# Optimization experiments

Hardware: AMD Instinct MI355X
Metric: run time of the kernel (lower is better)

Reference implementation:

```python
import jax, jax.numpy as jnp
import numpy as np

EMB = 64
N_NODES = 50000
N_EDGES = 800000

def _mlp(h, W1, b1, W2, b2):
    h = jax.nn.relu(h @ W1 + b1)
    return jax.nn.relu(h @ W2 + b2)

def setup_inputs() -> dict:
    key = jax.random.key(0)
    ks = jax.random.split(key, 12)
    s = 1.0 / np.sqrt(3 * EMB)
    s2 = 1.0 / np.sqrt(EMB)
    x = jax.random.normal(ks[0], (N_NODES, 2 * EMB), dtype=jnp.float32)
    edge_index = jax.random.randint(ks[1], (2, N_EDGES), 0, N_NODES, dtype=jnp.int32)
    edge_attr = jax.random.normal(ks[2], (N_EDGES, EMB), dtype=jnp.float32)
    u = jax.random.normal(ks[3], (64, 64), dtype=jnp.float32)
    batch = jax.random.randint(ks[4], (N_NODES,), 0, 64, dtype=jnp.int32)
    W1a = jax.random.uniform(ks[5], (3 * EMB, EMB), jnp.float32, -s, s)
    b1a = jax.random.uniform(ks[6], (EMB,), jnp.float32, -s, s)
    W1b = jax.random.uniform(ks[7], (EMB, EMB), jnp.float32, -s2, s2)
    b1b = jax.random.uniform(ks[8], (EMB,), jnp.float32, -s2, s2)
    W2a = jax.random.uniform(ks[9], (3 * EMB, EMB), jnp.float32, -s, s)
    b2a = jax.random.uniform(ks[10], (EMB,), jnp.float32, -s, s)
    W2b = jax.random.uniform(ks[11], (EMB, EMB), jnp.float32, -s2, s2)
    b2b = jax.random.uniform(jax.random.fold_in(key, 99), (EMB,), jnp.float32, -s2, s2)
    return {"x": x, "edge_index": edge_index, "edge_attr": edge_attr, "u": u, "batch": batch,
            "W1a": W1a, "b1a": b1a, "W1b": W1b, "b1b": b1b,
            "W2a": W2a, "b2a": b2a, "W2b": W2b, "b2b": b2b}

def reference(x, edge_index, edge_attr, u, batch, W1a, b1a, W1b, b1b, W2a, b2a, W2b, b2b):
    senders, receivers = edge_index[0], edge_index[1]
    # gather sender node features [E, 2*EMB] and concat edge features -> [E, 3*EMB]
    msg = jnp.concatenate([x[senders], edge_attr], axis=1)
    msg = _mlp(msg, W1a, b1a, W1b, b1b)  # [E, EMB]
    agg = jax.ops.segment_sum(msg, receivers, num_segments=x.shape[0])  # [N, EMB]
    h = jnp.concatenate([x, agg], axis=1)  # [N, 3*EMB]
    return _mlp(h, W2a, b2a, W2b, b2b)  # [N, EMB]
```

## Files before the change

kernel.cpp:

```cpp
#include <hip/hip_runtime.h>
#include <hip/hip_bf16.h>

typedef __attribute__((ext_vector_type(8))) __bf16 bf16x8;
typedef __attribute__((ext_vector_type(4))) __bf16 bf16x4;
typedef __attribute__((ext_vector_type(2))) __bf16 bf16x2;
typedef __attribute__((ext_vector_type(4))) float f32x4;

#define MFMA(a, b, c) __builtin_amdgcn_mfma_f32_16x16x32_bf16((a), (b), (c), 0, 0, 0)

__device__ __forceinline__ bf16x8 pack8(f32x4 a, f32x4 b) {
    bf16x8 r;
    r[0] = (__bf16)a[0]; r[1] = (__bf16)a[1]; r[2] = (__bf16)a[2]; r[3] = (__bf16)a[3];
    r[4] = (__bf16)b[0]; r[5] = (__bf16)b[1]; r[6] = (__bf16)b[2]; r[7] = (__bf16)b[3];
    return r;
}

__device__ __forceinline__ bf16x8 cvt8(const float* __restrict__ p) {
    return pack8(*(const f32x4*)(p), *(const f32x4*)(p + 4));
}

__global__ __launch_bounds__(256) void zero_i32(int* __restrict__ p, int n) {
    for (int i = blockIdx.x * blockDim.x + threadIdx.x; i < n;
         i += gridDim.x * blockDim.x)
        p[i] = 0;
}

__global__ __launch_bounds__(256) void precompute_y(
    const float* __restrict__ x,
    const float* __restrict__ W1a, const float* __restrict__ b1a,
    const float* __restrict__ W2a, const float* __restrict__ b2a,
    float* __restrict__ y1, float* __restrict__ y2,
    int N, int ntiles)
{
    const int LDK = 136;
    __shared__ __align__(16) __bf16 w1t[64 * 136];
    __shared__ __align__(16) __bf16 w2t[64 * 136];
    for (int idx = threadIdx.x; idx < 64 * 128; idx += 256) {
        int k = idx >> 6, n = idx & 63;
        w1t[n * LDK + k] = (__bf16)W1a[k * 64 + n];
        w2t[n * LDK + k] = (__bf16)W2a[k * 64 + n];
    }
    __syncthreads();

    const int lane = threadIdx.x & 63, wave = threadIdx.x >> 6;
    const int l15 = lane & 15, l4 = lane >> 4;

    f32x4 bias1[4], bias2[4];
#pragma unroll
    for (int nt = 0; nt < 4; ++nt) {
        bias1[nt] = *(const f32x4*)(b1a + nt * 16 + l4 * 4);
        bias2[nt] = *(const f32x4*)(b2a + nt * 16 + l4 * 4);
    }

    for (int tile = blockIdx.x * 4 + wave; tile < ntiles; tile += gridDim.x * 4) {
        const int node = tile * 16 + l15;
        const int nrow = min(node, N - 1);
        f32x4 acc1[4], acc2[4];
#pragma unroll
        for (int nt = 0; nt < 4; ++nt) {
            acc1[nt] = (f32x4){0.f, 0.f, 0.f, 0.f};
            acc2[nt] = (f32x4){0.f, 0.f, 0.f, 0.f};
        }
#pragma unroll
        for (int j = 0; j < 4; ++j) {
            const int k0 = j * 32 + l4 * 8;
            bf16x8 b = cvt8(x + (size_t)nrow * 128 + k0);
#pragma unroll
            for (int nt = 0; nt < 4; ++nt) {
                bf16x8 a1 = *(const bf16x8*)(w1t + (nt * 16 + l15) * LDK + k0);
                acc1[nt] = MFMA(a1, b, acc1[nt]);
                bf16x8 a2 = *(const bf16x8*)(w2t + (nt * 16 + l15) * LDK + k0);
                acc2[nt] = MFMA(a2, b, acc2[nt]);
            }
        }
        if (node < N) {
#pragma unroll
            for (int nt = 0; nt < 4; ++nt) {
                f32x4 v1 = acc1[nt] + bias1[nt];
                f32x4 v2 = acc2[nt] + bias2[nt];
                *(f32x4*)(y1 + (size_t)node * 64 + nt * 16 + l4 * 4) = v1;
                *(f32x4*)(y2 + (size_t)node * 64 + nt * 16 + l4 * 4) = v2;
            }
        }
    }
}

__global__ __launch_bounds__(256) void hist_rank(
    const int* __restrict__ recv, int* __restrict__ cnt,
    int* __restrict__ rank, int E)
{
    for (int e = blockIdx.x * blockDim.x + threadIdx.x; e < E;
         e += gridDim.x * blockDim.x)
        rank[e] = atomicAdd(&cnt[recv[e]], 1);
}

__global__ __launch_bounds__(1024) void scan_offsets(
    const int* __restrict__ cnt, int* __restrict__ offs, int N)
{
    __shared__ int wsum[16];
    __shared__ int stot;
    const int tid = threadIdx.x;
    const int lane = tid & 63, wave = tid >> 6;
    int carry = 0;
    const int CH = 4096;
    for (int base = 0; base < N; base += CH) {
        const int idx = base + tid * 4;
        int v0 = (idx + 0 < N) ? cnt[idx + 0] : 0;
        int v1 = (idx + 1 < N) ? cnt[idx + 1] : 0;
        int v2 = (idx + 2 < N) ? cnt[idx + 2] : 0;
        int v3 = (idx + 3 < N) ? cnt[idx + 3] : 0;
        const int t = v0 + v1 + v2 + v3;
        int s = t;
#pragma unroll
        for (int d = 1; d < 64; d <<= 1) {
            int u = __shfl_up(s, d);
            if (lane >= d) s += u;
        }
        if (lane == 63) wsum[wave] = s;
        __syncthreads();
        if (wave == 0) {
            int w = (lane < 16) ? wsum[lane] : 0;
            int ws = w;
#pragma unroll
            for (int d = 1; d < 16; d <<= 1) {
                int u = __shfl_up(ws, d);
                if (lane >= d) ws += u;
            }
            if (lane < 16) wsum[lane] = ws - w;
            if (lane == 15) stot = ws;
        }
        __syncthreads();
        const int excl = s - t + wsum[wave] + carry;
        if (idx + 0 < N) offs[idx + 0] = excl;
        if (idx + 1 < N) offs[idx + 1] = excl + v0;
        if (idx + 2 < N) offs[idx + 2] = excl + v0 + v1;
        if (idx + 3 < N) offs[idx + 3] = excl + v0 + v1 + v2;
        carry += stot;
        __syncthreads();
    }
    if (tid == 0) offs[N] = carry;
}

template<int MODE>
__global__ __launch_bounds__(256) void edge_mlp(
    const float* __restrict__ eattr,
    const int* __restrict__ send, const int* __restrict__ recv,
    const int* __restrict__ rank, const int* __restrict__ offs,
    const float* __restrict__ W1a, const float* __restrict__ W1b,
    const float* __restrict__ b1b,
    const float* __restrict__ y1,
    __bf16* __restrict__ msgC, float* agg,
    int E, int ntiles)
{
    __shared__ __align__(16) __bf16 wfA[8 * 65 * 8];
    __shared__ __align__(16) __bf16 wfB[8 * 65 * 8];
    __shared__ __align__(16) __bf16 hfrag[4][8 * 17 * 8];
    for (int idx = threadIdx.x; idx < 64 * 64; idx += 256) {
        const int k = idx >> 6, n = idx & 63;
        const int c = k >> 3, i = k & 7;
        wfA[(c * 65 + n) * 8 + i] = (__bf16)W1a[(128 + k) * 64 + n];
        wfB[(c * 65 + n) * 8 + i] = (__bf16)W1b[k * 64 + n];
    }
    __syncthreads();

    const int lane = threadIdx.x & 63, wave = threadIdx.x >> 6;
    const int l15 = lane & 15, l4 = lane >> 4;
    __bf16* hf = hfrag[wave];

    f32x4 biasb[4];
#pragma unroll
    for (int nt = 0; nt < 4; ++nt) biasb[nt] = *(const f32x4*)(b1b + nt * 16 + l4 * 4);

    for (int tile = blockIdx.x * 4 + wave; tile < ntiles; tile += gridDim.x * 4) {
        const int e = tile * 16 + l15;
        const int el = min(e, E - 1);
        const int s = send[el];
        int p = 0, rv = 0;
        if (MODE == 0) {
            rv = recv[el];
            p = offs[rv] + rank[el];
        } else {
            rv = recv[el];
        }

        f32x4 acc[4];
#pragma unroll
        for (int nt = 0; nt < 4; ++nt)
            acc[nt] = *(const f32x4*)(y1 + (size_t)s * 64 + nt * 16 + l4 * 4);
#pragma unroll
        for (int j = 0; j < 2; ++j) {
            const float* ep = eattr + (size_t)el * 64 + j * 32 + l4 * 8;
            bf16x8 b = pack8(*(const f32x4*)ep, *(const f32x4*)(ep + 4));
            const int c = j * 4 + l4;
#pragma unroll
            for (int nt = 0; nt < 4; ++nt) {
                bf16x8 a = *(const bf16x8*)(wfA + ((c * 65) + nt * 16 + l15) * 8);
                acc[nt] = MFMA(a, b, acc[nt]);
            }
        }
#pragma unroll
        for (int nt = 0; nt < 4; ++nt) {
            bf16x4 hv;
#pragma unroll
            for (int r = 0; r < 4; ++r) hv[r] = (__bf16)fmaxf(acc[nt][r], 0.f);
            const int c2 = nt * 2 + (l4 >> 1);
            *(bf16x4*)(hf + (c2 * 17 + l15) * 8 + (l4 & 1) * 4) = hv;
        }
        f32x4 acc2[4];
#pragma unroll
        for (int nt = 0; nt < 4; ++nt) acc2[nt] = biasb[nt];
#pragma unroll
        for (int j = 0; j < 2; ++j) {
            const int c = j * 4 + l4;
            bf16x8 b = *(const bf16x8*)(hf + (c * 17 + l15) * 8);
#pragma unroll
            for (int nt = 0; nt < 4; ++nt) {
                bf16x8 a = *(const bf16x8*)(wfB + ((c * 65) + nt * 16 + l15) * 8);
                acc2[nt] = MFMA(a, b, acc2[nt]);
            }
        }
        if (e < E) {
            if (MODE == 0) {
                __bf16* row = msgC + (size_t)p * 64;
#pragma unroll
                for (int nt = 0; nt < 4; ++nt) {
                    bf16x4 mv;
#pragma unroll
                    for (int r = 0; r < 4; ++r) mv[r] = (__bf16)fmaxf(acc2[nt][r], 0.f);
                    *(bf16x4*)(row + nt * 16 + l4 * 4) = mv;
                }
            } else {
                float* base = agg + (size_t)rv * 64 + l4 * 4;
#pragma unroll
                for (int nt = 0; nt < 4; ++nt)
#pragma unroll
                    for (int r = 0; r < 4; ++r)
                        unsafeAtomicAdd(base + nt * 16 + r, fmaxf(acc2[nt][r], 0.f));
            }
        }
    }
}

__global__ __launch_bounds__(256) void csr_reduce(
    const unsigned* __restrict__ msg_u,
    const int* __restrict__ offs,
    __bf16* __restrict__ aggB, int N)
{
    const int wave = threadIdx.x >> 6, lane = threadIdx.x & 63;
    const int half = lane >> 5, c = lane & 31;
    for (int node = blockIdx.x * 4 + wave; node < N; node += gridDim.x * 4) {
        const int oL = offs[node], oR = offs[node + 1];
        float ax = 0.f, ay = 0.f;
        for (int p = oL + half; p < oR; p += 2) {
            const unsigned u = msg_u[(size_t)p * 32 + c];
            ax += __uint_as_float(u << 16);
            ay += __uint_as_float(u & 0xffff0000u);
        }
        ax += __shfl_xor(ax, 32);
        ay += __shfl_xor(ay, 32);
        if (half == 0) {
            bf16x2 v; v[0] = (__bf16)ax; v[1] = (__bf16)ay;
            *(bf16x2*)(aggB + (size_t)node * 64 + c * 2) = v;
        }
    }
}

template<int AGGF32>
__global__ __launch_bounds__(256) void node_pass(
    const void* __restrict__ aggp,
    const float* __restrict__ W2a, const float* __restrict__ W2b,
    const float* __restrict__ b2b,
    const float* __restrict__ y2, float* __restrict__ out,
    int N, int ntiles)
{
    const int LDK = 72;
    __shared__ __align__(16) __bf16 wat[64 * 72];
    __shared__ __align__(16) __bf16 wbt[64 * 72];
    __shared__ __align__(16) __bf16 hbuf[4][16 * 72];
    for (int idx = threadIdx.x; idx < 64 * 64; idx += 256) {
        int k = idx >> 6, n = idx & 63;
        wat[n * LDK + k] = (__bf16)W2a[(128 + k) * 64 + n];
        wbt[n * LDK + k] = (__bf16)W2b[k * 64 + n];
    }
    __syncthreads();

    const int lane = threadIdx.x & 63, wave = threadIdx.x >> 6;
    const int l15 = lane & 15, l4 = lane >> 4;
    __bf16* hb = hbuf[wave];

    f32x4 biasb[4];
#pragma unroll
    for (int nt = 0; nt < 4; ++nt) biasb[nt] = *(const f32x4*)(b2b + nt * 16 + l4 * 4);

    for (int tile = blockIdx.x * 4 + wave; tile < ntiles; tile += gridDim.x * 4) {
        const int node = tile * 16 + l15;
        const int nrow = min(node, N - 1);

        f32x4 acc[4];
#pragma unroll
        for (int nt = 0; nt < 4; ++nt)
            acc[nt] = *(const f32x4*)(y2 + (size_t)nrow * 64 + nt * 16 + l4 * 4);
#pragma unroll
        for (int j = 0; j < 2; ++j) {
            const int k0 = j * 32 + l4 * 8;
            bf16x8 b;
            if (AGGF32) b = cvt8((const float*)aggp + (size_t)nrow * 64 + k0);
            else        b = *(const bf16x8*)((const __bf16*)aggp + (size_t)nrow * 64 + k0);
#pragma unroll
            for (int nt = 0; nt < 4; ++nt) {
                bf16x8 a = *(const bf16x8*)(wat + (nt * 16 + l15) * LDK + k0);
                acc[nt] = MFMA(a, b, acc[nt]);
            }
        }
#pragma unroll
        for (int nt = 0; nt < 4; ++nt) {
            bf16x4 hv;
#pragma unroll
            for (int r = 0; r < 4; ++r) hv[r] = (__bf16)fmaxf(acc[nt][r], 0.f);
            *(bf16x4*)(hb + l15 * LDK + nt * 16 + l4 * 4) = hv;
        }

        f32x4 acc2[4];
#pragma unroll
        for (int nt = 0; nt < 4; ++nt) acc2[nt] = biasb[nt];
#pragma unroll
        for (int j = 0; j < 2; ++j) {
            const int k0 = j * 32 + l4 * 8;
            bf16x8 b = *(const bf16x8*)(hb + l15 * LDK + k0);
#pragma unroll
            for (int nt = 0; nt < 4; ++nt) {
                bf16x8 a = *(const bf16x8*)(wbt + (nt * 16 + l15) * LDK + k0);
                acc2[nt] = MFMA(a, b, acc2[nt]);
            }
        }
        if (node < N) {
#pragma unroll
            for (int nt = 0; nt < 4; ++nt) {
                f32x4 v;
#pragma unroll
                for (int r = 0; r < 4; ++r) v[r] = fmaxf(acc2[nt][r], 0.f);
                *(f32x4*)(out + (size_t)node * 64 + nt * 16 + l4 * 4) = v;
            }
        }
    }
}

extern "C" void kernel_launch(void* const* d_in, const int* in_sizes, int n_in,
                              void* d_out, int out_size, void* d_ws, size_t ws_size,
                              hipStream_t stream) {
    const float* x     = (const float*)d_in[0];
    const int*   eidx  = (const int*)d_in[1];
    const float* eattr = (const float*)d_in[2];
    const float* W1a = (const float*)d_in[5];
    const float* b1a = (const float*)d_in[6];
    const float* W1b = (const float*)d_in[7];
    const float* b1b = (const float*)d_in[8];
    const float* W2a = (const float*)d_in[9];
    const float* b2a = (const float*)d_in[10];
    const float* W2b = (const float*)d_in[11];
    const float* b2b = (const float*)d_in[12];
    float* out = (float*)d_out;

    const int N = in_sizes[0] / 128;
    const int E = in_sizes[1] / 2;
    const int* send = eidx;
    const int* recv = eidx + E;

    const size_t NG = (size_t)N * 64;
    const size_t need = 2 * NG * sizeof(float) + (size_t)E * 64 * sizeof(__bf16)
                      + ((size_t)2 * (N + 1) + E) * sizeof(int);
    const bool big = ws_size >= need;

    const int ntilesN = (N + 15) / 16;
    const int ntilesE = (E + 15) / 16;
    int blkN = (ntilesN + 3) / 4;
    if (blkN > 1024) blkN = 1024;
    int blkE = (ntilesE + 3) / 4;
    if (blkE > 1536) blkE = 1536;
    int blkS = (E + 255) / 256;
    if (blkS > 1024) blkS = 1024;
    int blkR = (N + 3) / 4;
    if (blkR > 2048) blkR = 2048;

    if (big) {
        float*  y1   = (float*)d_ws;
        float*  y2   = y1 + NG;
        __bf16* msgC = (__bf16*)(y2 + NG);
        int*    cnt  = (int*)(msgC + (size_t)E * 64);
        int*    offs = cnt + (N + 1);
        int*    rank = offs + (N + 1);
        __bf16* aggB = (__bf16*)y1;

        zero_i32<<<(N + 256) / 256, 256, 0, stream>>>(cnt, N + 1);
        hist_rank<<<blkS, 256, 0, stream>>>(recv, cnt, rank, E);
        scan_offsets<<<1, 1024, 0, stream>>>(cnt, offs, N);
        precompute_y<<<blkN, 256, 0, stream>>>(x, W1a, b1a, W2a, b2a, y1, y2, N, ntilesN);
        edge_mlp<0><<<blkE, 256, 0, stream>>>(eattr, send, recv, rank, offs,
                                              W1a, W1b, b1b, y1, msgC, nullptr, E, ntilesE);
        csr_reduce<<<blkR, 256, 0, stream>>>((const unsigned*)msgC, offs, aggB, N);
        node_pass<0><<<blkN, 256, 0, stream>>>(aggB, W2a, W2b, b2b, y2, out, N, ntilesN);
    } else {
        float* agg = (float*)d_ws;
        float* y1  = agg + NG;
        float* y2  = y1 + NG;
        zero_i32<<<2048, 256, 0, stream>>>((int*)agg, (int)NG);
        precompute_y<<<blkN, 256, 0, stream>>>(x, W1a, b1a, W2a, b2a, y1, y2, N, ntilesN);
        edge_mlp<1><<<blkE, 256, 0, stream>>>(eattr, send, recv, nullptr, nullptr,
                                              W1a, W1b, b1b, y1, nullptr, agg, E, ntilesE);
        node_pass<1><<<blkN, 256, 0, stream>>>(agg, W2a, W2b, b2b, y2, out, N, ntilesN);
    }
}
```

Measured before the change: 243.9 us.

## Store y1 as bf16, transpose hidden via shuffles, fuse CSR reduce into node MLP

Stores the precomputed sender projection y1 in bf16, using a fragment-friendly layout that halves the random-gather traffic in the edge MLP. Replaces the LDS round-trip between the two MFMA layers with register shuffles in both edge and node kernels. Fuses the CSR segment reduction into the node MLP kernel, so the separate aggregation write and read and one launch go away. The costs are extra bf16 rounding of y1, more shuffle instructions, and a serial 16-node reduction loop per wave in the fused node kernel.

Result: slower. 302.0 us (+23.8%).

```diff
diff --git a/kernel.cpp b/kernel.cpp
--- a/kernel.cpp
+++ b/kernel.cpp
@@ -5,6 +5,7 @@
 typedef __attribute__((ext_vector_type(4))) __bf16 bf16x4;
 typedef __attribute__((ext_vector_type(2))) __bf16 bf16x2;
 typedef __attribute__((ext_vector_type(4))) float f32x4;
+typedef __attribute__((ext_vector_type(4))) unsigned u32x4;
 
 #define MFMA(a, b, c) __builtin_amdgcn_mfma_f32_16x16x32_bf16((a), (b), (c), 0, 0, 0)
 
@@ -19,6 +20,36 @@
     return pack8(*(const f32x4*)(p), *(const f32x4*)(p + 4));
 }
 
+__device__ __forceinline__ unsigned pkrelu(float a, float b) {
+    unsigned short ua = __builtin_bit_cast(unsigned short, (__bf16)fmaxf(a, 0.f));
+    unsigned short ub = __builtin_bit_cast(unsigned short, (__bf16)fmaxf(b, 0.f));
+    return (unsigned)ua | ((unsigned)ub << 16);
+}
+
+__device__ __forceinline__ void transpose_h(const f32x4* acc, bf16x8* bfr,
+                                            int l15, int l4) {
+    unsigned pk[4][2];
+#pragma unroll
+    for (int nt = 0; nt < 4; ++nt) {
+        pk[nt][0] = pkrelu(acc[nt][0], acc[nt][1]);
+        pk[nt][1] = pkrelu(acc[nt][2], acc[nt][3]);
+    }
+    const int srcA = l15 + 16 * ((2 * l4) & 3);
+    const int srcB = l15 + 16 * ((2 * l4 + 1) & 3);
+    const bool hi = (l4 >> 1) != 0;
+#pragma unroll
+    for (int j = 0; j < 2; ++j) {
+        unsigned a0 = __shfl(pk[j * 2][0], srcA), a1 = __shfl(pk[j * 2][1], srcA);
+        unsigned c0 = __shfl(pk[j * 2 + 1][0], srcA), c1 = __shfl(pk[j * 2 + 1][1], srcA);
+        unsigned b0 = __shfl(pk[j * 2][0], srcB), b1 = __shfl(pk[j * 2][1], srcB);
+        unsigned d0 = __shfl(pk[j * 2 + 1][0], srcB), d1 = __shfl(pk[j * 2 + 1][1], srcB);
+        u32x4 uv;
+        uv[0] = hi ? c0 : a0; uv[1] = hi ? c1 : a1;
+        uv[2] = hi ? d0 : b0; uv[3] = hi ? d1 : b1;
+        bfr[j] = __builtin_bit_cast(bf16x8, uv);
+    }
+}
+
 __global__ __launch_bounds__(256) void zero_i32(int* __restrict__ p, int n) {
     for (int i = blockIdx.x * blockDim.x + threadIdx.x; i < n;
          i += gridDim.x * blockDim.x)
@@ -29,7 +60,7 @@
     const float* __restrict__ x,
     const float* __restrict__ W1a, const float* __restrict__ b1a,
     const float* __restrict__ W2a, const float* __restrict__ b2a,
-    float* __restrict__ y1, float* __restrict__ y2,
+    __bf16* __restrict__ y1f, float* __restrict__ y2,
     int N, int ntiles)
 {
     const int LDK = 136;
@@ -77,8 +108,11 @@
 #pragma unroll
             for (int nt = 0; nt < 4; ++nt) {
                 f32x4 v1 = acc1[nt] + bias1[nt];
+                bf16x4 bv;
+#pragma unroll
+                for (int r = 0; r < 4; ++r) bv[r] = (__bf16)v1[r];
+                *(bf16x4*)(y1f + (size_t)node * 64 + l4 * 16 + nt * 4) = bv;
                 f32x4 v2 = acc2[nt] + bias2[nt];
-                *(f32x4*)(y1 + (size_t)node * 64 + nt * 16 + l4 * 4) = v1;
                 *(f32x4*)(y2 + (size_t)node * 64 + nt * 16 + l4 * 4) = v2;
             }
         }
@@ -148,13 +182,12 @@
     const int* __restrict__ rank, const int* __restrict__ offs,
     const float* __restrict__ W1a, const float* __restrict__ W1b,
     const float* __restrict__ b1b,
-    const float* __restrict__ y1,
+    const __bf16* __restrict__ y1f,
     __bf16* __restrict__ msgC, float* agg,
     int E, int ntiles)
 {
     __shared__ __align__(16) __bf16 wfA[8 * 65 * 8];
     __shared__ __align__(16) __bf16 wfB[8 * 65 * 8];
-    __shared__ __align__(16) __bf16 hfrag[4][8 * 17 * 8];
     for (int idx = threadIdx.x; idx < 64 * 64; idx += 256) {
         const int k = idx >> 6, n = idx & 63;
         const int c = k >> 3, i = k & 7;
@@ -165,7 +198,6 @@
 
     const int lane = threadIdx.x & 63, wave = threadIdx.x >> 6;
     const int l15 = lane & 15, l4 = lane >> 4;
-    __bf16* hf = hfrag[wave];
 
     f32x4 biasb[4];
 #pragma unroll
@@ -175,18 +207,20 @@
         const int e = tile * 16 + l15;
         const int el = min(e, E - 1);
         const int s = send[el];
-        int p = 0, rv = 0;
-        if (MODE == 0) {
-            rv = recv[el];
-            p = offs[rv] + rank[el];
-        } else {
-            rv = recv[el];
-        }
-
+        const int rv = recv[el];
+        int p = 0;
+        if (MODE == 0) p = offs[rv] + rank[el];
+
+        bf16x8 cA = *(const bf16x8*)(y1f + (size_t)s * 64 + l4 * 16);
+        bf16x8 cB = *(const bf16x8*)(y1f + (size_t)s * 64 + l4 * 16 + 8);
         f32x4 acc[4];
 #pragma unroll
-        for (int nt = 0; nt < 4; ++nt)
-            acc[nt] = *(const f32x4*)(y1 + (size_t)s * 64 + nt * 16 + l4 * 4);
+        for (int r = 0; r < 4; ++r) {
+            acc[0][r] = (float)cA[r];
+            acc[1][r] = (float)cA[4 + r];
+            acc[2][r] = (float)cB[r];
+            acc[3][r] = (float)cB[4 + r];
+        }
 #pragma unroll
         for (int j = 0; j < 2; ++j) {
             const float* ep = eattr + (size_t)el * 64 + j * 32 + l4 * 8;
@@ -198,25 +232,19 @@
                 acc[nt] = MFMA(a, b, acc[nt]);
             }
         }
-#pragma unroll
-        for (int nt = 0; nt < 4; ++nt) {
-            bf16x4 hv;
-#pragma unroll
-            for (int r = 0; r < 4; ++r) hv[r] = (__bf16)fmaxf(acc[nt][r], 0.f);
-            const int c2 = nt * 2 + (l4 >> 1);
-            *(bf16x4*)(hf + (c2 * 17 + l15) * 8 + (l4 & 1) * 4) = hv;
-        }
+        bf16x8 bfr[2];
+        transpose_h(acc, bfr, l15, l4);
+
         f32x4 acc2[4];
 #pragma unroll
         for (int nt = 0; nt < 4; ++nt) acc2[nt] = biasb[nt];
 #pragma unroll
         for (int j = 0; j < 2; ++j) {
             const int c = j * 4 + l4;
-            bf16x8 b = *(const bf16x8*)(hf + (c * 17 + l15) * 8);
 #pragma unroll
             for (int nt = 0; nt < 4; ++nt) {
                 bf16x8 a = *(const bf16x8*)(wfB + ((c * 65) + nt * 16 + l15) * 8);
-                acc2[nt] = MFMA(a, b, acc2[nt]);
+                acc2[nt] = MFMA(a, bfr[j], acc2[nt]);
             }
         }
         if (e < E) {
@@ -241,52 +269,117 @@
     }
 }
 
-__global__ __launch_bounds__(256) void csr_reduce(
+__global__ __launch_bounds__(256) void node_fused(
     const unsigned* __restrict__ msg_u,
     const int* __restrict__ offs,
-    __bf16* __restrict__ aggB, int N)
-{
-    const int wave = threadIdx.x >> 6, lane = threadIdx.x & 63;
-    const int half = lane >> 5, c = lane & 31;
-    for (int node = blockIdx.x * 4 + wave; node < N; node += gridDim.x * 4) {
-        const int oL = offs[node], oR = offs[node + 1];
-        float ax = 0.f, ay = 0.f;
-        for (int p = oL + half; p < oR; p += 2) {
-            const unsigned u = msg_u[(size_t)p * 32 + c];
-            ax += __uint_as_float(u << 16);
-            ay += __uint_as_float(u & 0xffff0000u);
-        }
-        ax += __shfl_xor(ax, 32);
-        ay += __shfl_xor(ay, 32);
-        if (half == 0) {
-            bf16x2 v; v[0] = (__bf16)ax; v[1] = (__bf16)ay;
-            *(bf16x2*)(aggB + (size_t)node * 64 + c * 2) = v;
-        }
-    }
-}
-
-template<int AGGF32>
-__global__ __launch_bounds__(256) void node_pass(
-    const void* __restrict__ aggp,
     const float* __restrict__ W2a, const float* __restrict__ W2b,
     const float* __restrict__ b2b,
     const float* __restrict__ y2, float* __restrict__ out,
     int N, int ntiles)
 {
-    const int LDK = 72;
-    __shared__ __align__(16) __bf16 wat[64 * 72];
-    __shared__ __align__(16) __bf16 wbt[64 * 72];
-    __shared__ __align__(16) __bf16 hbuf[4][16 * 72];
+    const int LDA = 72;
+    __shared__ __align__(16) __bf16 wfA[8 * 65 * 8];
+    __shared__ __align__(16) __bf16 wfB[8 * 65 * 8];
+    __shared__ __align__(16) __bf16 aggL[4][16 * 72];
     for (int idx = threadIdx.x; idx < 64 * 64; idx += 256) {
-        int k = idx >> 6, n = idx & 63;
-        wat[n * LDK + k] = (__bf16)W2a[(128 + k) * 64 + n];
-        wbt[n * LDK + k] = (__bf16)W2b[k * 64 + n];
+        const int k = idx >> 6, n = idx & 63;
+        const int c = k >> 3, i = k & 7;
+        wfA[(c * 65 + n) * 8 + i] = (__bf16)W2a[(128 + k) * 64 + n];
+        wfB[(c * 65 + n) * 8 + i] = (__bf16)W2b[k * 64 + n];
     }
     __syncthreads();
 
     const int lane = threadIdx.x & 63, wave = threadIdx.x >> 6;
     const int l15 = lane & 15, l4 = lane >> 4;
-    __bf16* hb = hbuf[wave];
+    const int half = lane >> 5, cc = lane & 31;
+    __bf16* aL = aggL[wave];
+
+    f32x4 biasb[4];
+#pragma unroll
+    for (int nt = 0; nt < 4; ++nt) biasb[nt] = *(const f32x4*)(b2b + nt * 16 + l4 * 4);
+
+    for (int tile = blockIdx.x * 4 + wave; tile < ntiles; tile += gridDim.x * 4) {
+        const int rbase = tile * 16;
+
+        for (int m = 0; m < 16; ++m) {
+            const int node = rbase + m;
+            const int oL = offs[min(node, N)], oR = offs[min(node + 1, N)];
+            float ax = 0.f, ay = 0.f;
+            for (int p = oL + half; p < oR; p += 2) {
+                const unsigned u = msg_u[(size_t)p * 32 + cc];
+                ax += __uint_as_float(u << 16);
+                ay += __uint_as_float(u & 0xffff0000u);
+            }
+            ax += __shfl_xor(ax, 32);
+            ay += __shfl_xor(ay, 32);
+            if (half == 0) {
+                bf16x2 v; v[0] = (__bf16)ax; v[1] = (__bf16)ay;
+                *(bf16x2*)(aL + m * LDA + cc * 2) = v;
+            }
+        }
+
+        const int node = rbase + l15;
+        const int nrow = min(node, N - 1);
+        f32x4 acc[4];
+#pragma unroll
+        for (int nt = 0; nt < 4; ++nt)
+            acc[nt] = *(const f32x4*)(y2 + (size_t)nrow * 64 + nt * 16 + l4 * 4);
+#pragma unroll
+        for (int j = 0; j < 2; ++j) {
+            bf16x8 b = *(const bf16x8*)(aL + l15 * LDA + j * 32 + l4 * 8);
+            const int c = j * 4 + l4;
+#pragma unroll
+            for (int nt = 0; nt < 4; ++nt) {
+                bf16x8 a = *(const bf16x8*)(wfA + ((c * 65) + nt * 16 + l15) * 8);
+                acc[nt] = MFMA(a, b, acc[nt]);
+            }
+        }
+        bf16x8 bfr[2];
+        transpose_h(acc, bfr, l15, l4);
+
+        f32x4 acc2[4];
+#pragma unroll
+        for (int nt = 0; nt < 4; ++nt) acc2[nt] = biasb[nt];
+#pragma unroll
+        for (int j = 0; j < 2; ++j) {
+            const int c = j * 4 + l4;
+#pragma unroll
+            for (int nt = 0; nt < 4; ++nt) {
+                bf16x8 a = *(const bf16x8*)(wfB + ((c * 65) + nt * 16 + l15) * 8);
+                acc2[nt] = MFMA(a, bfr[j], acc2[nt]);
+            }
+        }
+        if (node < N) {
+#pragma unroll
+            for (int nt = 0; nt < 4; ++nt) {
+                f32x4 v;
+#pragma unroll
+                for (int r = 0; r < 4; ++r) v[r] = fmaxf(acc2[nt][r], 0.f);
+                *(f32x4*)(out + (size_t)node * 64 + nt * 16 + l4 * 4) = v;
+            }
+        }
+    }
+}
+
+__global__ __launch_bounds__(256) void node_pass_f32(
+    const float* __restrict__ agg,
+    const float* __restrict__ W2a, const float* __restrict__ W2b,
+    const float* __restrict__ b2b,
+    const float* __restrict__ y2, float* __restrict__ out,
+    int N, int ntiles)
+{
+    __shared__ __align__(16) __bf16 wfA[8 * 65 * 8];
+    __shared__ __align__(16) __bf16 wfB[8 * 65 * 8];
+    for (int idx = threadIdx.x; idx < 64 * 64; idx += 256) {
+        const int k = idx >> 6, n = idx & 63;
+        const int c = k >> 3, i = k & 7;
+        wfA[(c * 65 + n) * 8 + i] = (__bf16)W2a[(128 + k) * 64 + n];
+        wfB[(c * 65 + n) * 8 + i] = (__bf16)W2b[k * 64 + n];
+    }
+    __syncthreads();
+
+    const int lane = threadIdx.x & 63, wave = threadIdx.x >> 6;
+    const int l15 = lane & 15, l4 = lane >> 4;
 
     f32x4 biasb[4];
 #pragma unroll
@@ -295,42 +388,32 @@
     for (int tile = blockIdx.x * 4 + wave; tile < ntiles; tile += gridDim.x * 4) {
         const int node = tile * 16 + l15;
         const int nrow = min(node, N - 1);
-
         f32x4 acc[4];
 #pragma unroll
         for (int nt = 0; nt < 4; ++nt)
             acc[nt] = *(const f32x4*)(y2 + (size_t)nrow * 64 + nt * 16 + l4 * 4);
 #pragma unroll
         for (int j = 0; j < 2; ++j) {
-            const int k0 = j * 32 + l4 * 8;
-            bf16x8 b;
-            if (AGGF32) b = cvt8((const float*)aggp + (size_t)nrow * 64 + k0);
-            else        b = *(const bf16x8*)((const __bf16*)aggp + (size_t)nrow * 64 + k0);
-#pragma unroll
-            for (int nt = 0; nt < 4; ++nt) {
-                bf16x8 a = *(const bf16x8*)(wat + (nt * 16 + l15) * LDK + k0);
+            bf16x8 b = cvt8(agg + (size_t)nrow * 64 + j * 32 + l4 * 8);
+            const int c = j * 4 + l4;
+#pragma unroll
+            for (int nt = 0; nt < 4; ++nt) {
+                bf16x8 a = *(const bf16x8*)(wfA + ((c * 65) + nt * 16 + l15) * 8);
                 acc[nt] = MFMA(a, b, acc[nt]);
             }
         }
-#pragma unroll
-        for (int nt = 0; nt < 4; ++nt) {
-            bf16x4 hv;
-#pragma unroll
-            for (int r = 0; r < 4; ++r) hv[r] = (__bf16)fmaxf(acc[nt][r], 0.f);
-            *(bf16x4*)(hb + l15 * LDK + nt * 16 + l4 * 4) = hv;
-        }
-
+        bf16x8 bfr[2];
+        transpose_h(acc, bfr, l15, l4);
         f32x4 acc2[4];
 #pragma unroll
         for (int nt = 0; nt < 4; ++nt) acc2[nt] = biasb[nt];
 #pragma unroll
         for (int j = 0; j < 2; ++j) {
-            const int k0 = j * 32 + l4 * 8;
-            bf16x8 b = *(const bf16x8*)(hb + l15 * LDK + k0);
-#pragma unroll
-            for (int nt = 0; nt < 4; ++nt) {
-                bf16x8 a = *(const bf16x8*)(wbt + (nt * 16 + l15) * LDK + k0);
-                acc2[nt] = MFMA(a, b, acc2[nt]);
+            const int c = j * 4 + l4;
+#pragma unroll
+            for (int nt = 0; nt < 4; ++nt) {
+                bf16x8 a = *(const bf16x8*)(wfB + ((c * 65) + nt * 16 + l15) * 8);
+                acc2[nt] = MFMA(a, bfr[j], acc2[nt]);
             }
         }
         if (node < N) {
@@ -367,7 +450,7 @@
     const int* recv = eidx + E;
 
     const size_t NG = (size_t)N * 64;
-    const size_t need = 2 * NG * sizeof(float) + (size_t)E * 64 * sizeof(__bf16)
+    const size_t need = NG * 2 + NG * 4 + (size_t)E * 64 * 2
                       + ((size_t)2 * (N + 1) + E) * sizeof(int);
     const bool big = ws_size >= need;
 
@@ -376,37 +459,36 @@
     int blkN = (ntilesN + 3) / 4;
     if (blkN > 1024) blkN = 1024;
     int blkE = (ntilesE + 3) / 4;
-    if (blkE > 1536) blkE = 1536;
+    if (blkE > 2048) blkE = 2048;
     int blkS = (E + 255) / 256;
     if (blkS > 1024) blkS = 1024;
-    int blkR = (N + 3) / 4;
-    if (blkR > 2048) blkR = 2048;
+    int blkF = (ntilesN + 3) / 4;
+    if (blkF > 1536) blkF = 1536;
 
     if (big) {
-        float*  y1   = (float*)d_ws;
-        float*  y2   = y1 + NG;
+        __bf16* y1f  = (__bf16*)d_ws;
+        float*  y2   = (float*)(y1f + NG);
         __bf16* msgC = (__bf16*)(y2 + NG);
         int*    cnt  = (int*)(msgC + (size_t)E * 64);
         int*    offs = cnt + (N + 1);
         int*    rank = offs + (N + 1);
-        __bf16* aggB = (__bf16*)y1;
 
         zero_i32<<<(N + 256) / 256, 256, 0, stream>>>(cnt, N + 1);
         hist_rank<<<blkS, 256, 0, stream>>>(recv, cnt, rank, E);
         scan_offsets<<<1, 1024, 0, stream>>>(cnt, offs, N);
-        precompute_y<<<blkN, 256, 0, stream>>>(x, W1a, b1a, W2a, b2a, y1, y2, N, ntilesN);
+        precompute_y<<<blkN, 256, 0, stream>>>(x, W1a, b1a, W2a, b2a, y1f, y2, N, ntilesN);
         edge_mlp<0><<<blkE, 256, 0, stream>>>(eattr, send, recv, rank, offs,
-                                              W1a, W1b, b1b, y1, msgC, nullptr, E, ntilesE);
-        csr_reduce<<<blkR, 256, 0, stream>>>((const unsigned*)msgC, offs, aggB, N);
-        node_pass<0><<<blkN, 256, 0, stream>>>(aggB, W2a, W2b, b2b, y2, out, N, ntilesN);
+                                              W1a, W1b, b1b, y1f, msgC, nullptr, E, ntilesE);
+        node_fused<<<blkF, 256, 0, stream>>>((const unsigned*)msgC, offs,
+                                             W2a, W2b, b2b, y2, out, N, ntilesN);
     } else {
-        float* agg = (float*)d_ws;
-        float* y1  = agg + NG;
-        float* y2  = y1 + NG;
+        float*  agg = (float*)d_ws;
+        __bf16* y1f = (__bf16*)(agg + NG);
+        float*  y2  = (float*)(y1f + NG);
         zero_i32<<<2048, 256, 0, stream>>>((int*)agg, (int)NG);
-        precompute_y<<<blkN, 256, 0, stream>>>(x, W1a, b1a, W2a, b2a, y1, y2, N, ntilesN);
+        precompute_y<<<blkN, 256, 0, stream>>>(x, W1a, b1a, W2a, b2a, y1f, y2, N, ntilesN);
         edge_mlp<1><<<blkE, 256, 0, stream>>>(eattr, send, recv, nullptr, nullptr,
-                                              W1a, W1b, b1b, y1, nullptr, agg, E, ntilesE);
-        node_pass<1><<<blkN, 256, 0, stream>>>(agg, W2a, W2b, b2b, y2, out, N, ntilesN);
-    }
-}
+                                              W1a, W1b, b1b, y1f, nullptr, agg, E, ntilesE);
+        node_pass_f32<<<blkN, 256, 0, stream>>>(agg, W2a, W2b, b2b, y2, out, N, ntilesN);
+    }
+}
```
